# Performance work log

Hardware: AMD Instinct MI355X
Metric: run time of the kernel (lower is better)

## Reference

```python
import jax, jax.numpy as jnp
import numpy as np

N = 100000   # nodes
E = 1600000  # edges (avg degree 16)
D = 64       # feature / hidden / embedding dim
OUT = 2
NEG_SLOPE = 0.2


def setup_inputs() -> dict:
    key = jax.random.key(0)
    ks = jax.random.split(key, 12)
    s = 1.0 / np.sqrt(D)
    return {
        "x": jax.random.normal(ks[0], (N, D), dtype=jnp.float32),
        "edge_index": jax.random.randint(ks[1], (2, E), 0, N, dtype=jnp.int64),
        "Wl": jax.random.normal(ks[2], (3, D, D), dtype=jnp.float32) * s,
        "bl": jnp.zeros((3, D), dtype=jnp.float32),
        "Wr": jax.random.normal(ks[3], (3, D, D), dtype=jnp.float32) * s,
        "br": jnp.zeros((3, D), dtype=jnp.float32),
        "att": jax.random.normal(ks[4], (3, D), dtype=jnp.float32) * s,
        "bg": jnp.zeros((3, D), dtype=jnp.float32),
        "Ws": jax.random.normal(ks[5], (3, D, D), dtype=jnp.float32) * s,
        "bs": jnp.zeros((3, D), dtype=jnp.float32),
        "Wout": jax.random.normal(ks[6], (D, OUT), dtype=jnp.float32) * s,
        "bout": jnp.zeros((OUT,), dtype=jnp.float32),
    }


def _gatv2(h, src, dst, Wl, bl, Wr, br, att, bg):
    # GATv2Conv (heads=1, concat, add_self_loops=False):
    #   e_ij = att . LeakyReLU(Wl h_j + Wr h_i); softmax over incoming edges of i;
    #   out_i = sum_j alpha_ij * (Wl h_j) + bias
    xl = h @ Wl + bl                      # [N, D] source transform
    xr = h @ Wr + br                      # [N, D] dest transform
    e = jax.nn.leaky_relu(xl[src] + xr[dst], NEG_SLOPE) @ att  # [E]
    m = jax.ops.segment_max(e, dst, num_segments=N)            # per-dest max
    a = jnp.exp(e - m[dst])                                    # [E]
    denom = jax.ops.segment_sum(a, dst, num_segments=N)        # [N]
    alpha = a / denom[dst]                                     # [E]
    agg = jax.ops.segment_sum(alpha[:, None] * xl[src], dst, num_segments=N)
    return agg + bg                                            # [N, D]


def reference(x, edge_index, Wl, bl, Wr, br, att, bg, Ws, bs, Wout, bout):
    src, dst = edge_index[0], edge_index[1]
    # layer 1: gat1 + skip1, relu (dropout_rate=0 -> identity)
    h = jax.nn.relu(_gatv2(x, src, dst, Wl[0], bl[0], Wr[0], br[0], att[0], bg[0])
                    + x @ Ws[0] + bs[0])
    # middle layer
    h = jax.nn.relu(_gatv2(h, src, dst, Wl[1], bl[1], Wr[1], br[1], att[1], bg[1])
                    + h @ Ws[1] + bs[1])
    # last gat layer: no relu after
    h = _gatv2(h, src, dst, Wl[2], bl[2], Wr[2], br[2], att[2], bg[2]) + h @ Ws[2] + bs[2]
    return h @ Wout + bout
```

## Files before the change

### kernel.cpp

```cpp
#include <hip/hip_runtime.h>
#include <stdint.h>

#define NN 100000
#define EE 1600000
#define DD 64
#define NBUCK 391
#define SCWG 200
#define SCCHUNK 8000

using short8 = __attribute__((ext_vector_type(8))) short;
using f32x4  = __attribute__((ext_vector_type(4))) float;
using f2     = __attribute__((ext_vector_type(2))) float;


__device__ __forceinline__ unsigned short bf16_rne(float f) {
    unsigned int u = __float_as_uint(f);
    unsigned int r = (u + 0x7FFFu + ((u >> 16) & 1u)) >> 16;
    return (unsigned short)r;
}
__device__ __forceinline__ float bf16_to_f32(unsigned short h) {
    return __uint_as_float(((unsigned int)h) << 16);
}


__global__ void bucket_hist(const int* __restrict__ dst, int* __restrict__ bhist) {
    __shared__ int h[NBUCK];
    int t = threadIdx.x;
    for (int b = t; b < NBUCK; b += 256) h[b] = 0;
    __syncthreads();
    int start = blockIdx.x * SCCHUNK;
    int endi = min(start + SCCHUNK, EE);
    for (int e = start + t; e < endi; e += 256)
        atomicAdd(&h[dst[e] >> 8], 1);
    __syncthreads();
    for (int b = t; b < NBUCK; b += 256)
        if (h[b]) atomicAdd(&bhist[b], h[b]);
}

__global__ void bucket_scan(const int* __restrict__ bhist, int* __restrict__ bbase,
                            int* __restrict__ bcursor, int* __restrict__ offsets) {
    __shared__ int s[512];
    int t = threadIdx.x;
    int v = (t < NBUCK) ? bhist[t] : 0;
    s[t] = v;
    __syncthreads();
    for (int off = 1; off < 512; off <<= 1) {
        int a = (t >= off) ? s[t - off] : 0;
        __syncthreads();
        s[t] += a;
        __syncthreads();
    }
    if (t < NBUCK) { int excl = s[t] - v; bbase[t] = excl; bcursor[t] = excl; }
    if (t == 0) { bbase[NBUCK] = EE; offsets[NN] = EE; }
}

__global__ void bucket_scatter(const int* __restrict__ src, const int* __restrict__ dst,
                               int* __restrict__ bcursor, unsigned int* __restrict__ bedges) {
    __shared__ int cnt[NBUCK];
    __shared__ int lcur[NBUCK];
    int t = threadIdx.x;
    for (int b = t; b < NBUCK; b += 256) cnt[b] = 0;
    __syncthreads();
    int start = blockIdx.x * SCCHUNK;
    int endi = min(start + SCCHUNK, EE);
    for (int e = start + t; e < endi; e += 256)
        atomicAdd(&cnt[dst[e] >> 8], 1);
    __syncthreads();
    for (int b = t; b < NBUCK; b += 256) {
        int c = cnt[b];
        lcur[b] = c ? atomicAdd(&bcursor[b], c) : 0;
    }
    __syncthreads();
    for (int e = start + t; e < endi; e += 256) {
        int d = dst[e];
        int pos = atomicAdd(&lcur[d >> 8], 1);
        bedges[pos] = ((unsigned int)(d & 255) << 24) | (unsigned int)src[e];
    }
}

__global__ void bucket_csr(const unsigned int* __restrict__ bedges, const int* __restrict__ bbase,
                           int* __restrict__ offsets, int* __restrict__ csr) {
    __shared__ int ncnt[256];
    __shared__ int lofs[256];
    int b = blockIdx.x;
    int t = threadIdx.x;
    int beg = bbase[b], endb = bbase[b + 1];
    ncnt[t] = 0;
    __syncthreads();
    for (int e = beg + t; e < endb; e += 256)
        atomicAdd(&ncnt[bedges[e] >> 24], 1);
    __syncthreads();
    int v = ncnt[t];
    lofs[t] = v;
    __syncthreads();
    for (int off = 1; off < 256; off <<= 1) {
        int a = (t >= off) ? lofs[t - off] : 0;
        __syncthreads();
        lofs[t] += a;
        __syncthreads();
    }
    int excl = lofs[t] - v;
    int node = b * 256 + t;
    if (node < NN) offsets[node] = beg + excl;
    __syncthreads();
    ncnt[t] = beg + excl;
    __syncthreads();
    for (int e = beg + t; e < endb; e += 256) {
        unsigned int ed = bedges[e];
        int pos = atomicAdd(&ncnt[ed >> 24], 1);
        csr[pos] = (int)(ed & 0xFFFFFFu);
    }
}


__global__ void conv_wx(const float* __restrict__ Wl, const float* __restrict__ Wr,
                        const float* __restrict__ Ws, const float* __restrict__ x,
                        unsigned short* __restrict__ Wt_hi, unsigned short* __restrict__ Wt_lo,
                        unsigned short* __restrict__ Ahi, unsigned short* __restrict__ Alo) {
    if (blockIdx.x < 144) {
        int e = blockIdx.x * 256 + threadIdx.x;
        if (e >= 9 * 4096) return;
        int mat = e >> 12;
        int r   = e & 4095;
        int k   = r >> 6, n = r & 63;
        int L = mat / 3, j = mat % 3;
        const float* W = (j == 0) ? Wl : ((j == 1) ? Wr : Ws);
        float v = W[L * 4096 + k * 64 + n];
        unsigned short hi = bf16_rne(v);
        unsigned short lo = bf16_rne(v - bf16_to_f32(hi));
        Wt_hi[mat * 4096 + n * 64 + k] = hi;
        Wt_lo[mat * 4096 + n * 64 + k] = lo;
    } else {
        int i = (blockIdx.x - 144) * 256 + threadIdx.x;
        int total = NN * 16;
        int stride = (gridDim.x - 144) * 256;
        for (; i < total; i += stride) {
            float4 v = *(const float4*)&x[(size_t)i * 4];
            ushort4 h, l;
            h.x = bf16_rne(v.x); l.x = bf16_rne(v.x - bf16_to_f32(h.x));
            h.y = bf16_rne(v.y); l.y = bf16_rne(v.y - bf16_to_f32(h.y));
            h.z = bf16_rne(v.z); l.z = bf16_rne(v.z - bf16_to_f32(h.z));
            h.w = bf16_rne(v.w); l.w = bf16_rne(v.w - bf16_to_f32(h.w));
            *(ushort4*)&Ahi[(size_t)i * 4] = h;
            *(ushort4*)&Alo[(size_t)i * 4] = l;
        }
    }
}


__global__ __launch_bounds__(256) void gemm_mfma(
    const unsigned short* __restrict__ Ahi, const unsigned short* __restrict__ Alo,
    const unsigned short* __restrict__ Wt_hi, const unsigned short* __restrict__ Wt_lo,
    const float* __restrict__ bl, const float* __restrict__ br, const float* __restrict__ bs,
    unsigned short* __restrict__ Xlb, unsigned short* __restrict__ XRS) {
    int lane = threadIdx.x & 63;
    int wid  = threadIdx.x >> 6;
    int m0 = (blockIdx.x * 4 + wid) * 32;
    if (m0 >= NN) return;

    int l4 = lane & 15;
    int hi = lane >> 4;
    int koff = hi * 8;

    int arow0 = m0 + l4, arow1 = m0 + 16 + l4;
    bool ok0 = arow0 < NN, ok1 = arow1 < NN;
    int ar0 = ok0 ? arow0 : NN - 1;
    int ar1 = ok1 ? arow1 : NN - 1;

    const unsigned short* ab0 = Ahi + (size_t)ar0 * 64;
    const unsigned short* lb0 = Alo + (size_t)ar0 * 64;
    const unsigned short* ab1 = Ahi + (size_t)ar1 * 64;
    const unsigned short* lb1 = Alo + (size_t)ar1 * 64;
    short8 a0hi0 = *(const short8*)(ab0 + koff);
    short8 a0hi1 = *(const short8*)(ab0 + 32 + koff);
    short8 a0lo0 = *(const short8*)(lb0 + koff);
    short8 a0lo1 = *(const short8*)(lb0 + 32 + koff);
    short8 a1hi0 = *(const short8*)(ab1 + koff);
    short8 a1hi1 = *(const short8*)(ab1 + 32 + koff);
    short8 a1lo0 = *(const short8*)(lb1 + koff);
    short8 a1lo1 = *(const short8*)(lb1 + 32 + koff);

    int nbase0 = hi * 4;

#pragma unroll
    for (int m = 0; m < 3; m++) {
        const unsigned short* wh = Wt_hi + m * 4096;
        const unsigned short* wl = Wt_lo + m * 4096;
        const float* bias = (m == 0) ? bl : ((m == 1) ? br : bs);
#pragma unroll
        for (int tt = 0; tt < 4; tt++) {
            int ncol = tt * 16 + l4;
            const unsigned short* bh = wh + ncol * 64 + koff;
            const unsigned short* blo = wl + ncol * 64 + koff;
            short8 bhi0 = *(const short8*)bh;
            short8 bhi1 = *(const short8*)(bh + 32);
            short8 blo0 = *(const short8*)blo;
            short8 blo1 = *(const short8*)(blo + 32);

            f32x4 acc0 = {0.f, 0.f, 0.f, 0.f};
            f32x4 acc1 = {0.f, 0.f, 0.f, 0.f};
            acc0 = __builtin_amdgcn_mfma_f32_16x16x32_bf16(bhi0, a0hi0, acc0, 0, 0, 0);
            acc1 = __builtin_amdgcn_mfma_f32_16x16x32_bf16(bhi0, a1hi0, acc1, 0, 0, 0);
            acc0 = __builtin_amdgcn_mfma_f32_16x16x32_bf16(bhi1, a0hi1, acc0, 0, 0, 0);
            acc1 = __builtin_amdgcn_mfma_f32_16x16x32_bf16(bhi1, a1hi1, acc1, 0, 0, 0);
            acc0 = __builtin_amdgcn_mfma_f32_16x16x32_bf16(blo0, a0hi0, acc0, 0, 0, 0);
            acc1 = __builtin_amdgcn_mfma_f32_16x16x32_bf16(blo0, a1hi0, acc1, 0, 0, 0);
            acc0 = __builtin_amdgcn_mfma_f32_16x16x32_bf16(blo1, a0hi1, acc0, 0, 0, 0);
            acc1 = __builtin_amdgcn_mfma_f32_16x16x32_bf16(blo1, a1hi1, acc1, 0, 0, 0);
            acc0 = __builtin_amdgcn_mfma_f32_16x16x32_bf16(bhi0, a0lo0, acc0, 0, 0, 0);
            acc1 = __builtin_amdgcn_mfma_f32_16x16x32_bf16(bhi0, a1lo0, acc1, 0, 0, 0);
            acc0 = __builtin_amdgcn_mfma_f32_16x16x32_bf16(bhi1, a0lo1, acc0, 0, 0, 0);
            acc1 = __builtin_amdgcn_mfma_f32_16x16x32_bf16(bhi1, a1lo1, acc1, 0, 0, 0);

            int nb = tt * 16 + nbase0;
            float4 bb = *(const float4*)&bias[nb];
            ushort4 h0, h1;
            h0.x = bf16_rne(acc0[0] + bb.x); h0.y = bf16_rne(acc0[1] + bb.y);
            h0.z = bf16_rne(acc0[2] + bb.z); h0.w = bf16_rne(acc0[3] + bb.w);
            h1.x = bf16_rne(acc1[0] + bb.x); h1.y = bf16_rne(acc1[1] + bb.y);
            h1.z = bf16_rne(acc1[2] + bb.z); h1.w = bf16_rne(acc1[3] + bb.w);
            if (m == 0) {
                if (ok0) *(ushort4*)&Xlb[(size_t)ar0 * 64 + nb] = h0;
                if (ok1) *(ushort4*)&Xlb[(size_t)ar1 * 64 + nb] = h1;
            } else {
                int coff = (m == 1) ? 0 : 64;
                if (ok0) *(ushort4*)&XRS[(size_t)ar0 * 128 + coff + nb] = h0;
                if (ok1) *(ushort4*)&XRS[(size_t)ar1 * 128 + coff + nb] = h1;
            }
        }
    }
}


__device__ __forceinline__ float group_sum16(float t) {
    t += __int_as_float(__builtin_amdgcn_update_dpp(0, __float_as_int(t), 0xB1, 0xF, 0xF, true));
    t += __int_as_float(__builtin_amdgcn_update_dpp(0, __float_as_int(t), 0x4E, 0xF, 0xF, true));
    t += __int_as_float(__builtin_amdgcn_update_dpp(0, __float_as_int(t), 0x141, 0xF, 0xF, true));
    t += __int_as_float(__builtin_amdgcn_update_dpp(0, __float_as_int(t), 0x140, 0xF, 0xF, true));
    return t;
}

__device__ __forceinline__ void unpack4(uint2 u, f2& v01, f2& v23) {
    v01 = f2{ __uint_as_float(u.x << 16), __uint_as_float(u.x & 0xFFFF0000u) };
    v23 = f2{ __uint_as_float(u.y << 16), __uint_as_float(u.y & 0xFFFF0000u) };
}

__global__ __launch_bounds__(256) void node_kernel(
    const unsigned short* __restrict__ Xlb, const unsigned short* __restrict__ XRS,
    const int* __restrict__ offsets, const int* __restrict__ csr,
    const float* __restrict__ att, const float* __restrict__ bg,
    unsigned short* __restrict__ houtHi, unsigned short* __restrict__ houtLo, int do_relu,
    const float* __restrict__ Wout, const float* __restrict__ bout,
    float* __restrict__ outp, int do_out) {
    int lane = threadIdx.x & 63;
    int wid  = threadIdx.x >> 6;
    int i = blockIdx.x * 4 + wid;
    if (i >= NN) return;
    int sub = lane & 15;
    int grp = lane >> 4;

    f2 xr01, xr23;
    unpack4(*(const uint2*)&XRS[(size_t)i * 128 + sub * 4], xr01, xr23);
    float4 att4 = *(const float4*)&att[sub * 4];
    f2 at01 = {att4.x, att4.y}, at23 = {att4.z, att4.w};

    f2 agg01 = {0.f, 0.f}, agg23 = {0.f, 0.f};
    float denom = 0.f;
    int beg = offsets[i], end = offsets[i + 1];

    for (int j0 = beg; j0 < end; j0 += 8) {
        int jA = j0 + grp, jB = jA + 4;
        bool vA = jA < end, vB = jB < end;
        int sA = csr[vA ? jA : beg];
        int sB = csr[vB ? jB : beg];
        uint2 uA = *(const uint2*)&Xlb[(size_t)sA * 64 + sub * 4];
        uint2 uB = *(const uint2*)&Xlb[(size_t)sB * 64 + sub * 4];
        f2 xA01, xA23, xB01, xB23;
        unpack4(uA, xA01, xA23);
        unpack4(uB, xB01, xB23);

        f2 sA01 = xA01 + xr01;
        f2 sA23 = xA23 + xr23;
        f2 sB01 = xB01 + xr01;
        f2 sB23 = xB23 + xr23;
        f2 lA01 = { fmaxf(sA01.x, 0.2f * sA01.x), fmaxf(sA01.y, 0.2f * sA01.y) };
        f2 lA23 = { fmaxf(sA23.x, 0.2f * sA23.x), fmaxf(sA23.y, 0.2f * sA23.y) };
        f2 lB01 = { fmaxf(sB01.x, 0.2f * sB01.x), fmaxf(sB01.y, 0.2f * sB01.y) };
        f2 lB23 = { fmaxf(sB23.x, 0.2f * sB23.x), fmaxf(sB23.y, 0.2f * sB23.y) };

        f2 tAv = lA01 * at01 + lA23 * at23;
        f2 tBv = lB01 * at01 + lB23 * at23;
        float tA = group_sum16(tAv.x + tAv.y);
        float tB = group_sum16(tBv.x + tBv.y);
        float aA = vA ? __expf(tA) : 0.f;
        float aB = vB ? __expf(tB) : 0.f;

        f2 aAv = {aA, aA};
        f2 aBv = {aB, aB};
        agg01 += aAv * xA01 + aBv * xB01;
        agg23 += aAv * xA23 + aBv * xB23;
        denom += aA + aB;
    }

    float aggx = agg01.x, aggy = agg01.y, aggz = agg23.x, aggw = agg23.y;
#pragma unroll
    for (int m = 16; m <= 32; m <<= 1) {
        aggx  += __shfl_xor(aggx, m, 64);
        aggy  += __shfl_xor(aggy, m, 64);
        aggz  += __shfl_xor(aggz, m, 64);
        aggw  += __shfl_xor(aggw, m, 64);
        denom += __shfl_xor(denom, m, 64);
    }

    float inv = (denom > 0.f) ? (1.0f / denom) : 0.f;
    f2 sk01, sk23;
    unpack4(*(const uint2*)&XRS[(size_t)i * 128 + 64 + sub * 4], sk01, sk23);
    float4 bg4 = *(const float4*)&bg[sub * 4];
    float4 res;
    res.x = aggx * inv + bg4.x + sk01.x;
    res.y = aggy * inv + bg4.y + sk01.y;
    res.z = aggz * inv + bg4.z + sk23.x;
    res.w = aggw * inv + bg4.w + sk23.y;
    if (do_relu) {
        res.x = fmaxf(res.x, 0.f); res.y = fmaxf(res.y, 0.f);
        res.z = fmaxf(res.z, 0.f); res.w = fmaxf(res.w, 0.f);
    }
    if (do_out) {
        float4 w01 = *(const float4*)&Wout[8 * sub];
        float4 w23 = *(const float4*)&Wout[8 * sub + 4];
        float o0 = res.x * w01.x + res.y * w01.z + res.z * w23.x + res.w * w23.z;
        float o1 = res.x * w01.y + res.y * w01.w + res.z * w23.y + res.w * w23.w;
        o0 = group_sum16(o0);
        o1 = group_sum16(o1);
        if (lane == 0) {
            outp[(size_t)i * 2 + 0] = o0 + bout[0];
            outp[(size_t)i * 2 + 1] = o1 + bout[1];
        }
    } else {
        if (grp == 0) {
            ushort4 h, l;
            h.x = bf16_rne(res.x); l.x = bf16_rne(res.x - bf16_to_f32(h.x));
            h.y = bf16_rne(res.y); l.y = bf16_rne(res.y - bf16_to_f32(h.y));
            h.z = bf16_rne(res.z); l.z = bf16_rne(res.z - bf16_to_f32(h.z));
            h.w = bf16_rne(res.w); l.w = bf16_rne(res.w - bf16_to_f32(h.w));
            *(ushort4*)&houtHi[(size_t)i * 64 + sub * 4] = h;
            *(ushort4*)&houtLo[(size_t)i * 64 + sub * 4] = l;
        }
    }
}


extern "C" void kernel_launch(void* const* d_in, const int* in_sizes, int n_in,
                              void* d_out, int out_size, void* d_ws, size_t ws_size,
                              hipStream_t stream) {
    const float* x    = (const float*)d_in[0];
    const int*   ei   = (const int*)d_in[1];
    const float* Wl   = (const float*)d_in[2];
    const float* bl   = (const float*)d_in[3];
    const float* Wr   = (const float*)d_in[4];
    const float* br   = (const float*)d_in[5];
    const float* att  = (const float*)d_in[6];
    const float* bg   = (const float*)d_in[7];
    const float* Ws   = (const float*)d_in[8];
    const float* bs   = (const float*)d_in[9];
    const float* Wout = (const float*)d_in[10];
    const float* bout = (const float*)d_in[11];
    float* out = (float*)d_out;

    size_t off = 0;
    char* base = (char*)d_ws;
    auto alloc = [&](size_t bytes) -> void* {
        void* p = base + off;
        off += (bytes + 255) & ~(size_t)255;
        return p;
    };
    unsigned short* Xlb = (unsigned short*)alloc((size_t)NN * 64 * 2);
    unsigned short* XRS = (unsigned short*)alloc((size_t)NN * 128 * 2);
    unsigned short* Ahi = (unsigned short*)alloc((size_t)NN * 64 * 2);
    unsigned short* Alo = (unsigned short*)alloc((size_t)NN * 64 * 2);
    unsigned short* Bhi = (unsigned short*)alloc((size_t)NN * 64 * 2);
    unsigned short* Blo = (unsigned short*)alloc((size_t)NN * 64 * 2);
    unsigned short* Wthi = (unsigned short*)alloc((size_t)9 * 4096 * 2);
    unsigned short* Wtlo = (unsigned short*)alloc((size_t)9 * 4096 * 2);
    int*  bhist  = (int*)alloc((size_t)NBUCK * 4);
    int*  bbase  = (int*)alloc((size_t)(NBUCK + 1) * 4);
    int*  bcur   = (int*)alloc((size_t)NBUCK * 4);
    unsigned int* bedges = (unsigned int*)alloc((size_t)EE * 4);
    int*  offs   = (int*)alloc((size_t)(NN + 1) * 4);
    int*  csr    = (int*)alloc((size_t)EE * 4);

    const int* src = ei;
    const int* dst = ei + EE;

    hipMemsetAsync(bhist, 0, (size_t)NBUCK * 4, stream);
    bucket_hist<<<SCWG, 256, 0, stream>>>(dst, bhist);
    bucket_scan<<<1, 512, 0, stream>>>(bhist, bbase, bcur, offs);
    bucket_scatter<<<SCWG, 256, 0, stream>>>(src, dst, bcur, bedges);
    bucket_csr<<<NBUCK, 256, 0, stream>>>(bedges, bbase, offs, csr);

    conv_wx<<<144 + 400, 256, 0, stream>>>(Wl, Wr, Ws, x, Wthi, Wtlo, Ahi, Alo);

    unsigned short* curHi = Ahi; unsigned short* curLo = Alo;
    unsigned short* nxtHi = Bhi; unsigned short* nxtLo = Blo;
    for (int L = 0; L < 3; L++) {
        gemm_mfma<<<(NN + 127) / 128, 256, 0, stream>>>(
            curHi, curLo, Wthi + (size_t)L * 3 * 4096, Wtlo + (size_t)L * 3 * 4096,
            bl + L * 64, br + L * 64, bs + L * 64, Xlb, XRS);
        node_kernel<<<NN / 4, 256, 0, stream>>>(
            Xlb, XRS, offs, csr, att + L * 64, bg + L * 64,
            nxtHi, nxtLo, (L < 2) ? 1 : 0,
            Wout, bout, out, (L == 2) ? 1 : 0);
        unsigned short* th = curHi; curHi = nxtHi; nxtHi = th;
        unsigned short* tl = curLo; curLo = nxtLo; nxtLo = tl;
    }
}
```

Baseline: 351.1 us.

## Drop low-half bf16 split of activations and refine CSR bucket granularity

The activations feeding each layer's GEMM are now stored as a single bf16 array instead of a hi/lo bf16 pair. This removes the lo-activation loads and writes and a third of the MFMA work, while the weights keep their hi/lo split. The CSR build switches to 128-node buckets, with more and smaller scatter chunks and a 1024-thread scan. The activation change costs accuracy, since activations are now truncated to bf16 precision.

```diff
diff --git a/kernel.cpp b/kernel.cpp
--- a/kernel.cpp
+++ b/kernel.cpp
@@ -4,9 +4,9 @@
 #define NN 100000
 #define EE 1600000
 #define DD 64
-#define NBUCK 391
-#define SCWG 200
-#define SCCHUNK 8000
+#define NBUCK 782
+#define SCWG 800
+#define SCCHUNK 2000
 
 using short8 = __attribute__((ext_vector_type(8))) short;
 using f32x4  = __attribute__((ext_vector_type(4))) float;
@@ -31,7 +31,7 @@
     int start = blockIdx.x * SCCHUNK;
     int endi = min(start + SCCHUNK, EE);
     for (int e = start + t; e < endi; e += 256)
-        atomicAdd(&h[dst[e] >> 8], 1);
+        atomicAdd(&h[dst[e] >> 7], 1);
     __syncthreads();
     for (int b = t; b < NBUCK; b += 256)
         if (h[b]) atomicAdd(&bhist[b], h[b]);
@@ -39,12 +39,12 @@
 
 __global__ void bucket_scan(const int* __restrict__ bhist, int* __restrict__ bbase,
                             int* __restrict__ bcursor, int* __restrict__ offsets) {
-    __shared__ int s[512];
+    __shared__ int s[1024];
     int t = threadIdx.x;
     int v = (t < NBUCK) ? bhist[t] : 0;
     s[t] = v;
     __syncthreads();
-    for (int off = 1; off < 512; off <<= 1) {
+    for (int off = 1; off < 1024; off <<= 1) {
         int a = (t >= off) ? s[t - off] : 0;
         __syncthreads();
         s[t] += a;
@@ -64,7 +64,7 @@
     int start = blockIdx.x * SCCHUNK;
     int endi = min(start + SCCHUNK, EE);
     for (int e = start + t; e < endi; e += 256)
-        atomicAdd(&cnt[dst[e] >> 8], 1);
+        atomicAdd(&cnt[dst[e] >> 7], 1);
     __syncthreads();
     for (int b = t; b < NBUCK; b += 256) {
         int c = cnt[b];
@@ -73,37 +73,40 @@
     __syncthreads();
     for (int e = start + t; e < endi; e += 256) {
         int d = dst[e];
-        int pos = atomicAdd(&lcur[d >> 8], 1);
-        bedges[pos] = ((unsigned int)(d & 255) << 24) | (unsigned int)src[e];
+        int pos = atomicAdd(&lcur[d >> 7], 1);
+        bedges[pos] = ((unsigned int)(d & 127) << 24) | (unsigned int)src[e];
     }
 }
 
 __global__ void bucket_csr(const unsigned int* __restrict__ bedges, const int* __restrict__ bbase,
                            int* __restrict__ offsets, int* __restrict__ csr) {
-    __shared__ int ncnt[256];
-    __shared__ int lofs[256];
+    __shared__ int ncnt[128];
+    __shared__ int lofs[128];
     int b = blockIdx.x;
     int t = threadIdx.x;
     int beg = bbase[b], endb = bbase[b + 1];
-    ncnt[t] = 0;
+    if (t < 128) ncnt[t] = 0;
     __syncthreads();
     for (int e = beg + t; e < endb; e += 256)
         atomicAdd(&ncnt[bedges[e] >> 24], 1);
     __syncthreads();
-    int v = ncnt[t];
-    lofs[t] = v;
-    __syncthreads();
-    for (int off = 1; off < 256; off <<= 1) {
-        int a = (t >= off) ? lofs[t - off] : 0;
+    if (t < 128) lofs[t] = ncnt[t];
+    __syncthreads();
+    for (int off = 1; off < 128; off <<= 1) {
+        int a = 0;
+        if (t < 128 && t >= off) a = lofs[t - off];
         __syncthreads();
-        lofs[t] += a;
+        if (t < 128) lofs[t] += a;
         __syncthreads();
     }
-    int excl = lofs[t] - v;
-    int node = b * 256 + t;
-    if (node < NN) offsets[node] = beg + excl;
-    __syncthreads();
-    ncnt[t] = beg + excl;
+    int excl = 0;
+    if (t < 128) {
+        excl = lofs[t] - ncnt[t];
+        int node = b * 128 + t;
+        if (node < NN) offsets[node] = beg + excl;
+    }
+    __syncthreads();
+    if (t < 128) ncnt[t] = beg + excl;
     __syncthreads();
     for (int e = beg + t; e < endb; e += 256) {
         unsigned int ed = bedges[e];
@@ -116,7 +119,7 @@
 __global__ void conv_wx(const float* __restrict__ Wl, const float* __restrict__ Wr,
                         const float* __restrict__ Ws, const float* __restrict__ x,
                         unsigned short* __restrict__ Wt_hi, unsigned short* __restrict__ Wt_lo,
-                        unsigned short* __restrict__ Ahi, unsigned short* __restrict__ Alo) {
+                        unsigned short* __restrict__ Ahi) {
     if (blockIdx.x < 144) {
         int e = blockIdx.x * 256 + threadIdx.x;
         if (e >= 9 * 4096) return;
@@ -136,20 +139,19 @@
         int stride = (gridDim.x - 144) * 256;
         for (; i < total; i += stride) {
             float4 v = *(const float4*)&x[(size_t)i * 4];
-            ushort4 h, l;
-            h.x = bf16_rne(v.x); l.x = bf16_rne(v.x - bf16_to_f32(h.x));
-            h.y = bf16_rne(v.y); l.y = bf16_rne(v.y - bf16_to_f32(h.y));
-            h.z = bf16_rne(v.z); l.z = bf16_rne(v.z - bf16_to_f32(h.z));
-            h.w = bf16_rne(v.w); l.w = bf16_rne(v.w - bf16_to_f32(h.w));
+            ushort4 h;
+            h.x = bf16_rne(v.x);
+            h.y = bf16_rne(v.y);
+            h.z = bf16_rne(v.z);
+            h.w = bf16_rne(v.w);
             *(ushort4*)&Ahi[(size_t)i * 4] = h;
-            *(ushort4*)&Alo[(size_t)i * 4] = l;
         }
     }
 }
 
 
 __global__ __launch_bounds__(256) void gemm_mfma(
-    const unsigned short* __restrict__ Ahi, const unsigned short* __restrict__ Alo,
+    const unsigned short* __restrict__ Ahi,
     const unsigned short* __restrict__ Wt_hi, const unsigned short* __restrict__ Wt_lo,
     const float* __restrict__ bl, const float* __restrict__ br, const float* __restrict__ bs,
     unsigned short* __restrict__ Xlb, unsigned short* __restrict__ XRS) {
@@ -168,17 +170,11 @@
     int ar1 = ok1 ? arow1 : NN - 1;
 
     const unsigned short* ab0 = Ahi + (size_t)ar0 * 64;
-    const unsigned short* lb0 = Alo + (size_t)ar0 * 64;
     const unsigned short* ab1 = Ahi + (size_t)ar1 * 64;
-    const unsigned short* lb1 = Alo + (size_t)ar1 * 64;
-    short8 a0hi0 = *(const short8*)(ab0 + koff);
-    short8 a0hi1 = *(const short8*)(ab0 + 32 + koff);
-    short8 a0lo0 = *(const short8*)(lb0 + koff);
-    short8 a0lo1 = *(const short8*)(lb0 + 32 + koff);
-    short8 a1hi0 = *(const short8*)(ab1 + koff);
-    short8 a1hi1 = *(const short8*)(ab1 + 32 + koff);
-    short8 a1lo0 = *(const short8*)(lb1 + koff);
-    short8 a1lo1 = *(const short8*)(lb1 + 32 + koff);
+    short8 a0k0 = *(const short8*)(ab0 + koff);
+    short8 a0k1 = *(const short8*)(ab0 + 32 + koff);
+    short8 a1k0 = *(const short8*)(ab1 + koff);
+    short8 a1k1 = *(const short8*)(ab1 + 32 + koff);
 
     int nbase0 = hi * 4;
 
@@ -199,18 +195,14 @@
 
             f32x4 acc0 = {0.f, 0.f, 0.f, 0.f};
             f32x4 acc1 = {0.f, 0.f, 0.f, 0.f};
-            acc0 = __builtin_amdgcn_mfma_f32_16x16x32_bf16(bhi0, a0hi0, acc0, 0, 0, 0);
-            acc1 = __builtin_amdgcn_mfma_f32_16x16x32_bf16(bhi0, a1hi0, acc1, 0, 0, 0);
-            acc0 = __builtin_amdgcn_mfma_f32_16x16x32_bf16(bhi1, a0hi1, acc0, 0, 0, 0);
-            acc1 = __builtin_amdgcn_mfma_f32_16x16x32_bf16(bhi1, a1hi1, acc1, 0, 0, 0);
-            acc0 = __builtin_amdgcn_mfma_f32_16x16x32_bf16(blo0, a0hi0, acc0, 0, 0, 0);
-            acc1 = __builtin_amdgcn_mfma_f32_16x16x32_bf16(blo0, a1hi0, acc1, 0, 0, 0);
-            acc0 = __builtin_amdgcn_mfma_f32_16x16x32_bf16(blo1, a0hi1, acc0, 0, 0, 0);
-            acc1 = __builtin_amdgcn_mfma_f32_16x16x32_bf16(blo1, a1hi1, acc1, 0, 0, 0);
-            acc0 = __builtin_amdgcn_mfma_f32_16x16x32_bf16(bhi0, a0lo0, acc0, 0, 0, 0);
-            acc1 = __builtin_amdgcn_mfma_f32_16x16x32_bf16(bhi0, a1lo0, acc1, 0, 0, 0);
-            acc0 = __builtin_amdgcn_mfma_f32_16x16x32_bf16(bhi1, a0lo1, acc0, 0, 0, 0);
-            acc1 = __builtin_amdgcn_mfma_f32_16x16x32_bf16(bhi1, a1lo1, acc1, 0, 0, 0);
+            acc0 = __builtin_amdgcn_mfma_f32_16x16x32_bf16(bhi0, a0k0, acc0, 0, 0, 0);
+            acc1 = __builtin_amdgcn_mfma_f32_16x16x32_bf16(bhi0, a1k0, acc1, 0, 0, 0);
+            acc0 = __builtin_amdgcn_mfma_f32_16x16x32_bf16(bhi1, a0k1, acc0, 0, 0, 0);
+            acc1 = __builtin_amdgcn_mfma_f32_16x16x32_bf16(bhi1, a1k1, acc1, 0, 0, 0);
+            acc0 = __builtin_amdgcn_mfma_f32_16x16x32_bf16(blo0, a0k0, acc0, 0, 0, 0);
+            acc1 = __builtin_amdgcn_mfma_f32_16x16x32_bf16(blo0, a1k0, acc1, 0, 0, 0);
+            acc0 = __builtin_amdgcn_mfma_f32_16x16x32_bf16(blo1, a0k1, acc0, 0, 0, 0);
+            acc1 = __builtin_amdgcn_mfma_f32_16x16x32_bf16(blo1, a1k1, acc1, 0, 0, 0);
 
             int nb = tt * 16 + nbase0;
             float4 bb = *(const float4*)&bias[nb];
@@ -249,7 +241,7 @@
     const unsigned short* __restrict__ Xlb, const unsigned short* __restrict__ XRS,
     const int* __restrict__ offsets, const int* __restrict__ csr,
     const float* __restrict__ att, const float* __restrict__ bg,
-    unsigned short* __restrict__ houtHi, unsigned short* __restrict__ houtLo, int do_relu,
+    unsigned short* __restrict__ hout, int do_relu,
     const float* __restrict__ Wout, const float* __restrict__ bout,
     float* __restrict__ outp, int do_out) {
     int lane = threadIdx.x & 63;
@@ -338,13 +330,12 @@
         }
     } else {
         if (grp == 0) {
-            ushort4 h, l;
-            h.x = bf16_rne(res.x); l.x = bf16_rne(res.x - bf16_to_f32(h.x));
-            h.y = bf16_rne(res.y); l.y = bf16_rne(res.y - bf16_to_f32(h.y));
-            h.z = bf16_rne(res.z); l.z = bf16_rne(res.z - bf16_to_f32(h.z));
-            h.w = bf16_rne(res.w); l.w = bf16_rne(res.w - bf16_to_f32(h.w));
-            *(ushort4*)&houtHi[(size_t)i * 64 + sub * 4] = h;
-            *(ushort4*)&houtLo[(size_t)i * 64 + sub * 4] = l;
+            ushort4 h;
+            h.x = bf16_rne(res.x);
+            h.y = bf16_rne(res.y);
+            h.z = bf16_rne(res.z);
+            h.w = bf16_rne(res.w);
+            *(ushort4*)&hout[(size_t)i * 64 + sub * 4] = h;
         }
     }
 }
@@ -377,9 +368,7 @@
     unsigned short* Xlb = (unsigned short*)alloc((size_t)NN * 64 * 2);
     unsigned short* XRS = (unsigned short*)alloc((size_t)NN * 128 * 2);
     unsigned short* Ahi = (unsigned short*)alloc((size_t)NN * 64 * 2);
-    unsigned short* Alo = (unsigned short*)alloc((size_t)NN * 64 * 2);
     unsigned short* Bhi = (unsigned short*)alloc((size_t)NN * 64 * 2);
-    unsigned short* Blo = (unsigned short*)alloc((size_t)NN * 64 * 2);
     unsigned short* Wthi = (unsigned short*)alloc((size_t)9 * 4096 * 2);
     unsigned short* Wtlo = (unsigned short*)alloc((size_t)9 * 4096 * 2);
     int*  bhist  = (int*)alloc((size_t)NBUCK * 4);
@@ -394,23 +383,22 @@
 
     hipMemsetAsync(bhist, 0, (size_t)NBUCK * 4, stream);
     bucket_hist<<<SCWG, 256, 0, stream>>>(dst, bhist);
-    bucket_scan<<<1, 512, 0, stream>>>(bhist, bbase, bcur, offs);
+    bucket_scan<<<1, 1024, 0, stream>>>(bhist, bbase, bcur, offs);
     bucket_scatter<<<SCWG, 256, 0, stream>>>(src, dst, bcur, bedges);
     bucket_csr<<<NBUCK, 256, 0, stream>>>(bedges, bbase, offs, csr);
 
-    conv_wx<<<144 + 400, 256, 0, stream>>>(Wl, Wr, Ws, x, Wthi, Wtlo, Ahi, Alo);
-
-    unsigned short* curHi = Ahi; unsigned short* curLo = Alo;
-    unsigned short* nxtHi = Bhi; unsigned short* nxtLo = Blo;
+    conv_wx<<<144 + 400, 256, 0, stream>>>(Wl, Wr, Ws, x, Wthi, Wtlo, Ahi);
+
+    unsigned short* cur = Ahi;
+    unsigned short* nxt = Bhi;
     for (int L = 0; L < 3; L++) {
         gemm_mfma<<<(NN + 127) / 128, 256, 0, stream>>>(
-            curHi, curLo, Wthi + (size_t)L * 3 * 4096, Wtlo + (size_t)L * 3 * 4096,
+            cur, Wthi + (size_t)L * 3 * 4096, Wtlo + (size_t)L * 3 * 4096,
             bl + L * 64, br + L * 64, bs + L * 64, Xlb, XRS);
         node_kernel<<<NN / 4, 256, 0, stream>>>(
             Xlb, XRS, offs, csr, att + L * 64, bg + L * 64,
-            nxtHi, nxtLo, (L < 2) ? 1 : 0,
+            nxt, (L < 2) ? 1 : 0,
             Wout, bout, out, (L == 2) ? 1 : 0);
-        unsigned short* th = curHi; curHi = nxtHi; nxtHi = th;
-        unsigned short* tl = curLo; curLo = nxtLo; nxtLo = tl;
-    }
-}
+        unsigned short* tp = cur; cur = nxt; nxt = tp;
+    }
+}
```

New measurement: 356.4 us. Within noise of the previous version (+1.5%).
